# Kernel tuning notes

Measured on AMD Instinct MI355X. Metric: run time of the kernel, lower is better.

## Reference

```python
import jax, jax.numpy as jnp
import numpy as np

N_NODES = 49984   # 32 graphs x 1562 nodes
N_EDGES = 799744  # avg degree 16
DIM_IN = 64
WIDTH = 256
DEPTH = 3         # depth+1 = 4 GCNConv blocks
N_GRAPHS = 32
NODES_PER_GRAPH = 1562


def setup_inputs() -> dict:
    key = jax.random.key(0)
    ks = jax.random.split(key, 12)
    nb = DEPTH + 1
    s_f = 1.0 / np.sqrt(DIM_IN)
    s_g = 1.0 / np.sqrt(WIDTH)
    return {
        "x": jax.random.normal(ks[0], (N_NODES, DIM_IN), dtype=jnp.float32),
        "edge_index": jax.random.randint(ks[1], (2, N_EDGES), 0, N_NODES, dtype=jnp.int32),
        "center": jax.random.randint(ks[2], (N_GRAPHS,), 0, NODES_PER_GRAPH, dtype=jnp.int32),
        "ptr": jnp.arange(N_GRAPHS + 1, dtype=jnp.int32) * NODES_PER_GRAPH,
        # foot: Conv1d(dim_input, width, 1) == per-node linear
        "Wf": jax.random.uniform(ks[3], (WIDTH, DIM_IN), jnp.float32, -s_f, s_f),
        "bf": jax.random.uniform(ks[4], (WIDTH,), jnp.float32, -s_f, s_f),
        # stacked GCNConv params: weight [nb, width, width] (in->out), bias [nb, width]
        "Wg": jax.random.uniform(ks[5], (nb, WIDTH, WIDTH), jnp.float32, -s_g, s_g),
        "bg": jax.random.uniform(ks[6], (nb, WIDTH), jnp.float32, -s_g, s_g),
        # head: Conv1d(width, 7, 1)
        "Wh": jax.random.uniform(ks[7], (7, WIDTH), jnp.float32, -s_g, s_g),
        "bh": jax.random.uniform(ks[8], (7,), jnp.float32, -s_g, s_g),
    }


def reference(x, edge_index, center, ptr, Wf, bf, Wg, bg, Wh, bh):
    N = x.shape[0]
    # foot: 1x1 conv (per-node linear) + exact GELU; dropout = identity (eval)
    h = jax.nn.gelu(x @ Wf.T + bf, approximate=False)  # [N, W]

    # gcn_norm with self-loops (same for every layer since edges are static)
    loops = jnp.arange(N, dtype=edge_index.dtype)
    row = jnp.concatenate([edge_index[0], loops])  # source
    col = jnp.concatenate([edge_index[1], loops])  # target
    deg = jax.ops.segment_sum(jnp.ones_like(row, dtype=h.dtype), col, num_segments=N)
    dis = jnp.where(deg > 0, jax.lax.rsqrt(jnp.maximum(deg, 1.0)), 0.0)
    norm = dis[row] * dis[col]  # [E+N]

    for l in range(Wg.shape[0]):
        xl = h @ Wg[l]                                   # [N, W] linear transform
        msg = xl[row] * norm[:, None]                    # gather + edge scale
        agg = jax.ops.segment_sum(msg, col, num_segments=N) + bg[l]
        h = h + agg                                      # residual

    out = jax.nn.gelu(h, approximate=False) @ Wh.T + bh  # [N, 7]
    return out[center + ptr[:-1]]                        # [B, 7]
```

## Files before the change

### kernel.cpp

```cpp
#include <hip/hip_runtime.h>
#include <math.h>

#define WIDTH 256
typedef unsigned short u16;
typedef unsigned int u32;
typedef __attribute__((ext_vector_type(4))) float f32x4;
typedef __attribute__((ext_vector_type(8))) short bf16x8;

__device__ __forceinline__ float gelu_exact(float v) {
    return 0.5f * v * (1.0f + erff(v * 0.70710678118654752f));
}
__device__ __forceinline__ u16 f2b(float x) {
    u32 u = __builtin_bit_cast(u32, x);
    return (u16)((u + 0x7fffu + ((u >> 16) & 1u)) >> 16);
}
__device__ __forceinline__ float b2f_lo(u32 v) {
    return __builtin_bit_cast(float, v << 16);
}
__device__ __forceinline__ float b2f_hi(u32 v) {
    return __builtin_bit_cast(float, v & 0xffff0000u);
}
__device__ __forceinline__ float b2fu(u16 b) {
    return __builtin_bit_cast(float, ((u32)b) << 16);
}
__device__ __forceinline__ u32 pack2(float a, float b) {
    return (u32)f2b(a) | ((u32)f2b(b) << 16);
}

#define PREP_WG   (4 * 65536)
#define PREP_WF   (256 * 64)
__global__ void k_prep(const float* __restrict__ Wg, const float* __restrict__ Wf,
                       const float* __restrict__ x,
                       u16* __restrict__ WgT, u16* __restrict__ WfT,
                       u16* __restrict__ xb, int total8) {
    int idx = blockIdx.x * blockDim.x + threadIdx.x;
    if (idx < PREP_WG) {
        int l = idx >> 16;
        int k = (idx >> 8) & 255;
        int n = idx & 255;
        WgT[(size_t)l * 65536 + (size_t)n * 256 + k] = f2b(Wg[idx]);
    } else if (idx < PREP_WG + PREP_WF) {
        int j = idx - PREP_WG;
        WfT[j] = f2b(Wf[j]);
    } else if (idx < PREP_WG + PREP_WF + total8) {
        int i = idx - (PREP_WG + PREP_WF);
        const float4 v0 = *reinterpret_cast<const float4*>(&x[(size_t)i * 8]);
        const float4 v1 = *reinterpret_cast<const float4*>(&x[(size_t)i * 8 + 4]);
        uint4 o;
        o.x = pack2(v0.x, v0.y);
        o.y = pack2(v0.z, v0.w);
        o.z = pack2(v1.x, v1.y);
        o.w = pack2(v1.z, v1.w);
        *reinterpret_cast<uint4*>(&xb[(size_t)i * 8]) = o;
    }
}

__global__ void k_hist(const int* __restrict__ col, int* __restrict__ deg,
                       u16* __restrict__ rank, int E) {
    int i = blockIdx.x * blockDim.x + threadIdx.x;
    if (i < E) rank[i] = (u16)atomicAdd(&deg[col[i]], 1);
}

__global__ __launch_bounds__(256) void k_scan1(const int* __restrict__ deg, int* __restrict__ off,
                                               int* __restrict__ part, float* __restrict__ dis, int N) {
    __shared__ int buf[256];
    const int t = threadIdx.x;
    const int gid = blockIdx.x * 256 + t;
    const int v = (gid < N) ? deg[gid] : 0;
    if (gid < N) dis[gid] = rsqrtf(1.0f + (float)v);
    buf[t] = v;
    __syncthreads();
#pragma unroll
    for (int d = 1; d < 256; d <<= 1) {
        int add = (t >= d) ? buf[t - d] : 0;
        __syncthreads();
        buf[t] += add;
        __syncthreads();
    }
    if (gid < N) off[gid] = buf[t] - v;
    if (t == 255) part[blockIdx.x] = buf[255];
}

__global__ __launch_bounds__(256) void k_scan3(int* __restrict__ off, const int* __restrict__ part,
                                               int NB, int N, int E) {
    __shared__ int buf[256];
    const int t = threadIdx.x;
    int v = (t < NB) ? part[t] : 0;
    buf[t] = v;
    __syncthreads();
#pragma unroll
    for (int d = 1; d < 256; d <<= 1) {
        int add = (t >= d) ? buf[t - d] : 0;
        __syncthreads();
        buf[t] += add;
        __syncthreads();
    }
    const int base = (blockIdx.x == 0) ? 0 : buf[blockIdx.x - 1];
    const int gid = blockIdx.x * 256 + t;
    if (gid < N) off[gid] += base;
    if (gid == 0) off[N] = E;
}

__global__ void k_fill(const int* __restrict__ row, const int* __restrict__ col,
                       const u16* __restrict__ rank, const float* __restrict__ dis,
                       const int* __restrict__ off, u32* __restrict__ csr, int E) {
    int i = blockIdx.x * blockDim.x + threadIdx.x;
    if (i < E) {
        const int r = row[i];
        const int pos = off[col[i]] + (int)rank[i];
        csr[pos] = (u32)(u16)r | ((u32)f2b(dis[r]) << 16);
    }
}

__global__ void k_front(const int* __restrict__ center, const int* __restrict__ ptr,
                        const int* __restrict__ off, const u32* __restrict__ csr,
                        int* __restrict__ flags, int* __restrict__ list, int* __restrict__ cnt) {
    const int g = blockIdx.x;
    const int node = center[g] + ptr[g];
    const int t = threadIdx.x;
    const int e0 = off[node];
    const int e1 = off[node + 1];
    if (t == 0) {
        if (atomicExch(&flags[node], 1) == 0) list[atomicAdd(cnt, 1)] = node;
    }
    for (int e = e0 + t; e < e1; e += 256) {
        const int s = (int)(csr[e] & 0xffffu);
        if (atomicExch(&flags[s], 1) == 0) list[atomicAdd(cnt, 1)] = s;
    }
}

template <int KDIM, bool FOOT>
__global__ __launch_bounds__(512) void k_gemm_mfma(const u16* __restrict__ A,
                                                   const u16* __restrict__ BT,
                                                   const float* __restrict__ bias,
                                                   u16* __restrict__ Cb,
                                                   float* __restrict__ Cf, int nrows) {
    __shared__ u16 As[128 * 64];
    __shared__ u16 Bs[256 * 64];

    const int tid = threadIdx.x;
    const int w = tid >> 6;
    const int l = tid & 63;
    const int m0 = blockIdx.x * 128;
    const int wr = w >> 2;
    const int wc = w & 3;

    const int lr = l >> 3;
    const int lc = l & 7;
    const int src_slot = lc ^ lr;

    f32x4 acc[4][4] = {};

#pragma unroll
    for (int ks = 0; ks < KDIM / 64; ++ks) {
        const int k0 = ks * 64;
#pragma unroll
        for (int i = 0; i < 2; ++i) {
            const u16* asrc = A + (size_t)(m0 + 16 * w + 8 * i + lr) * KDIM + k0 + src_slot * 8;
            __builtin_amdgcn_global_load_lds(
                (const __attribute__((address_space(1))) u32*)asrc,
                (__attribute__((address_space(3))) u32*)(As + (16 * w + 8 * i) * 64), 16, 0, 0);
        }
#pragma unroll
        for (int j = 0; j < 4; ++j) {
            const u16* bsrc = BT + (size_t)(32 * w + 8 * j + lr) * KDIM + k0 + src_slot * 8;
            __builtin_amdgcn_global_load_lds(
                (const __attribute__((address_space(1))) u32*)bsrc,
                (__attribute__((address_space(3))) u32*)(Bs + (32 * w + 8 * j) * 64), 16, 0, 0);
        }
        asm volatile("s_waitcnt vmcnt(0)" ::: "memory");
        __syncthreads();

        bf16x8 a[4][2], b[4][2];
#pragma unroll
        for (int fr = 0; fr < 4; ++fr) {
            const int row = 64 * wr + fr * 16 + (l & 15);
#pragma unroll
            for (int kk = 0; kk < 2; ++kk)
                a[fr][kk] = *reinterpret_cast<const bf16x8*>(
                    &As[row * 64 + ((kk * 4 + (l >> 4)) ^ (row & 7)) * 8]);
        }
#pragma unroll
        for (int fc = 0; fc < 4; ++fc) {
            const int row = 64 * wc + fc * 16 + (l & 15);
#pragma unroll
            for (int kk = 0; kk < 2; ++kk)
                b[fc][kk] = *reinterpret_cast<const bf16x8*>(
                    &Bs[row * 64 + ((kk * 4 + (l >> 4)) ^ (row & 7)) * 8]);
        }
#pragma unroll
        for (int fr = 0; fr < 4; ++fr)
#pragma unroll
            for (int fc = 0; fc < 4; ++fc) {
                acc[fr][fc] = __builtin_amdgcn_mfma_f32_16x16x32_bf16(a[fr][0], b[fc][0], acc[fr][fc], 0, 0, 0);
                acc[fr][fc] = __builtin_amdgcn_mfma_f32_16x16x32_bf16(a[fr][1], b[fc][1], acc[fr][fc], 0, 0, 0);
            }
        __syncthreads();
    }

    const int r0 = (l >> 4) * 4;
    const int ci = l & 15;
#pragma unroll
    for (int fr = 0; fr < 4; ++fr)
#pragma unroll
        for (int fc = 0; fc < 4; ++fc) {
            const int col = 64 * wc + fc * 16 + ci;
#pragma unroll
            for (int r = 0; r < 4; ++r) {
                const int row = m0 + 64 * wr + fr * 16 + r0 + r;
                if (row < nrows) {
                    const size_t p = (size_t)row * WIDTH + col;
                    if (FOOT) {
                        const float o = gelu_exact(acc[fr][fc][r] + bias[col]);
                        Cf[p] = o;
                        Cb[p] = f2b(o);
                    } else {
                        Cb[p] = f2b(acc[fr][fc][r]);
                    }
                }
            }
        }
}

#define EDGE_FMA(vv, dd_)                          \
    acc[0] = fmaf(dd_, b2f_lo(vv.x), acc[0]);      \
    acc[1] = fmaf(dd_, b2f_hi(vv.x), acc[1]);      \
    acc[2] = fmaf(dd_, b2f_lo(vv.y), acc[2]);      \
    acc[3] = fmaf(dd_, b2f_hi(vv.y), acc[3]);

__device__ __forceinline__ void agg_node_body(const int* __restrict__ off,
                                              const u32* __restrict__ csr,
                                              const float* __restrict__ dis,
                                              const u16* __restrict__ xlb,
                                              const float* __restrict__ bg,
                                              float* __restrict__ h,
                                              u16* __restrict__ hb,
                                              int node, int hl, int ch0) {
    const int c = ch0 + hl * 4;
    const int e0 = off[node];
    const int e1 = off[node + 1];
    const float di = dis[node];

    float acc[4];
    {
        const uint2 v = *reinterpret_cast<const uint2*>(&xlb[(size_t)node * WIDTH + c]);
        acc[0] = di * b2f_lo(v.x);
        acc[1] = di * b2f_hi(v.x);
        acc[2] = di * b2f_lo(v.y);
        acc[3] = di * b2f_hi(v.y);
    }

    for (int base = e0; base < e1; base += 32) {
        const int m = min(32, e1 - base);
        u32 ep = 0;
        if (hl < m) ep = csr[base + hl];
        int j = 0;
        for (; j + 8 <= m; j += 8) {
            uint2 vv[8];
            float dd[8];
#pragma unroll
            for (int q = 0; q < 8; ++q) {
                const u32 e = (u32)__shfl((int)ep, j + q, 32);
                dd[q] = b2f_hi(e);
                vv[q] = *reinterpret_cast<const uint2*>(&xlb[(size_t)(e & 0xffffu) * WIDTH + c]);
            }
#pragma unroll
            for (int q = 0; q < 8; ++q) { EDGE_FMA(vv[q], dd[q]) }
        }
        if (j + 4 <= m) {
            uint2 vv[4];
            float dd[4];
#pragma unroll
            for (int q = 0; q < 4; ++q) {
                const u32 e = (u32)__shfl((int)ep, j + q, 32);
                dd[q] = b2f_hi(e);
                vv[q] = *reinterpret_cast<const uint2*>(&xlb[(size_t)(e & 0xffffu) * WIDTH + c]);
            }
#pragma unroll
            for (int q = 0; q < 4; ++q) { EDGE_FMA(vv[q], dd[q]) }
            j += 4;
        }
        for (; j < m; ++j) {
            const u32 e = (u32)__shfl((int)ep, j, 32);
            const float dj = b2f_hi(e);
            const uint2 v = *reinterpret_cast<const uint2*>(&xlb[(size_t)(e & 0xffffu) * WIDTH + c]);
            EDGE_FMA(v, dj)
        }
    }

    const size_t p = (size_t)node * WIDTH + c;
    const float4 hv = *reinterpret_cast<const float4*>(&h[p]);
    const float4 bv = *reinterpret_cast<const float4*>(&bg[c]);
    const float o0 = hv.x + bv.x + di * acc[0];
    const float o1 = hv.y + bv.y + di * acc[1];
    const float o2 = hv.z + bv.z + di * acc[2];
    const float o3 = hv.w + bv.w + di * acc[3];
    float4 w0;
    w0.x = o0; w0.y = o1; w0.z = o2; w0.w = o3;
    *reinterpret_cast<float4*>(&h[p]) = w0;
    uint2 ob;
    ob.x = pack2(o0, o1);
    ob.y = pack2(o2, o3);
    *reinterpret_cast<uint2*>(&hb[p]) = ob;
}

__global__ __launch_bounds__(256) void k_agg(const int* __restrict__ off,
                                             const u32* __restrict__ csr,
                                             const float* __restrict__ dis,
                                             const u16* __restrict__ xlb,
                                             const float* __restrict__ bg,
                                             float* __restrict__ h,
                                             u16* __restrict__ hb, int nbh, int N) {
    int bh = blockIdx.x;
    int ch0 = 0;
    if (bh >= nbh) { ch0 = 128; bh -= nbh; }
    const int node = (bh * 256 + threadIdx.x) >> 5;
    if (node >= N) return;
    agg_node_body(off, csr, dis, xlb, bg, h, hb, node, threadIdx.x & 31, ch0);
}

__global__ __launch_bounds__(256) void k_agg_list(const int* __restrict__ off,
                                                  const u32* __restrict__ csr,
                                                  const float* __restrict__ dis,
                                                  const u16* __restrict__ xlb,
                                                  const float* __restrict__ bg,
                                                  float* __restrict__ h,
                                                  u16* __restrict__ hb,
                                                  const int* __restrict__ list,
                                                  const int* __restrict__ cnt) {
    const int nitems = cnt[0] * 2;
    const int hl = threadIdx.x & 31;
    const int stride = (gridDim.x * 256) >> 5;
    for (int item = (blockIdx.x * 256 + threadIdx.x) >> 5; item < nitems; item += stride) {
        const int node = list[item >> 1];
        const int ch0 = (item & 1) << 7;
        agg_node_body(off, csr, dis, xlb, bg, h, hb, node, hl, ch0);
    }
}
#undef EDGE_FMA

__global__ __launch_bounds__(256) void k_tail(const int* __restrict__ off,
                                              const u32* __restrict__ csr,
                                              const float* __restrict__ dis,
                                              const u16* __restrict__ hb,
                                              const float* __restrict__ h,
                                              const float* __restrict__ Wg3,
                                              const float* __restrict__ bg3,
                                              const float* __restrict__ Wh,
                                              const float* __restrict__ bh,
                                              const int* __restrict__ center,
                                              const int* __restrict__ ptr,
                                              float* __restrict__ out) {
    __shared__ float aggK[256];
    __shared__ u32 es[256];
    __shared__ float gs[256];
    const int g = blockIdx.x;
    const int t = threadIdx.x;
    const int node = center[g] + ptr[g];
    const int e0 = off[node];
    const int e1 = off[node + 1];
    const float di = dis[node];

    float acc = di * b2fu(hb[(size_t)node * WIDTH + t]);
    for (int base = e0; base < e1; base += 256) {
        const int m = min(256, e1 - base);
        if (t < m) es[t] = csr[base + t];
        __syncthreads();
        int j = 0;
        for (; j + 4 <= m; j += 4) {
            const u32 a0 = es[j + 0], a1 = es[j + 1], a2 = es[j + 2], a3 = es[j + 3];
            const float v0 = b2fu(hb[(size_t)(a0 & 0xffffu) * WIDTH + t]);
            const float v1 = b2fu(hb[(size_t)(a1 & 0xffffu) * WIDTH + t]);
            const float v2 = b2fu(hb[(size_t)(a2 & 0xffffu) * WIDTH + t]);
            const float v3 = b2fu(hb[(size_t)(a3 & 0xffffu) * WIDTH + t]);
            acc = fmaf(b2f_hi(a0), v0, acc);
            acc = fmaf(b2f_hi(a1), v1, acc);
            acc = fmaf(b2f_hi(a2), v2, acc);
            acc = fmaf(b2f_hi(a3), v3, acc);
        }
        for (; j < m; ++j) {
            const u32 a = es[j];
            acc = fmaf(b2f_hi(a), b2fu(hb[(size_t)(a & 0xffffu) * WIDTH + t]), acc);
        }
        __syncthreads();
    }
    aggK[t] = acc;
    __syncthreads();

    float mv = 0.0f;
#pragma unroll 8
    for (int k = 0; k < 256; ++k)
        mv = fmaf(aggK[k], Wg3[(size_t)k * 256 + t], mv);
    const float h4 = h[(size_t)node * WIDTH + t] + bg3[t] + di * mv;
    gs[t] = gelu_exact(h4);
    __syncthreads();
    if (t < 7) {
        float o = bh[t];
        for (int k = 0; k < 256; ++k)
            o = fmaf(gs[k], Wh[t * 256 + k], o);
        out[g * 7 + t] = o;
    }
}

extern "C" void kernel_launch(void* const* d_in, const int* in_sizes, int n_in,
                              void* d_out, int out_size, void* d_ws, size_t ws_size,
                              hipStream_t stream) {
    const float* x      = (const float*)d_in[0];
    const int*   ei     = (const int*)d_in[1];
    const int*   center = (const int*)d_in[2];
    const int*   ptr    = (const int*)d_in[3];
    const float* Wf     = (const float*)d_in[4];
    const float* bf     = (const float*)d_in[5];
    const float* Wg     = (const float*)d_in[6];
    const float* bg     = (const float*)d_in[7];
    const float* Wh     = (const float*)d_in[8];
    const float* bh     = (const float*)d_in[9];

    const int E = in_sizes[1] / 2;
    const int N = in_sizes[0] / 64;
    const int B = in_sizes[2];

    char* ws = (char*)d_ws;
    size_t o = 0;
    float* h       = (float*)(ws + o); o += (size_t)N * WIDTH * 4;
    u16*   hb      = (u16*)  (ws + o); o += (size_t)N * WIDTH * 2;
    u16*   xlb     = (u16*)  (ws + o); o += (size_t)N * WIDTH * 2;
    u16*   xb      = (u16*)  (ws + o); o += (size_t)N * 64 * 2;
    float* dis     = (float*)(ws + o); o += (size_t)N * 4;
    int*   deg     = (int*)  (ws + o); o += (size_t)N * 4;
    int*   off     = (int*)  (ws + o); o += (size_t)(N + 1) * 4;
    int*   part    = (int*)  (ws + o); o += 1024;
    u16*   rank    = (u16*)  (ws + o); o += (size_t)E * 2;
    u32*   csr     = (u32*)  (ws + o); o += (size_t)E * 4;
    u16*   WgT     = (u16*)  (ws + o); o += (size_t)4 * 65536 * 2;
    u16*   WfT     = (u16*)  (ws + o); o += (size_t)256 * 64 * 2;
    int*   flags   = (int*)  (ws + o); o += (size_t)N * 4;
    int*   cnt     = (int*)  (ws + o); o += 256;
    int*   list    = (int*)  (ws + o); o += (size_t)(E + 64) * 4;

    const int* rowv = ei;
    const int* colv = ei + E;

    const int nb = (N + 255) / 256;
    const int eb = (E + 255) / 256;

    hipMemsetAsync(deg, 0, (size_t)N * 4, stream);
    hipMemsetAsync(flags, 0, (size_t)N * 4 + 256, stream);
    const int total8 = N * 64 / 8;
    const int prep_threads = PREP_WG + PREP_WF + total8;
    k_prep<<<(prep_threads + 255) / 256, 256, 0, stream>>>(Wg, Wf, x, WgT, WfT, xb, total8);
    k_hist<<<eb, 256, 0, stream>>>(colv, deg, rank, E);
    k_scan1<<<nb, 256, 0, stream>>>(deg, off, part, dis, N);
    k_scan3<<<nb, 256, 0, stream>>>(off, part, nb, N, E);
    k_fill<<<eb, 256, 0, stream>>>(rowv, colv, rank, dis, off, csr, E);
    k_front<<<B, 256, 0, stream>>>(center, ptr, off, csr, flags, list, cnt);

    const int gb = (N + 127) / 128;
    k_gemm_mfma<64, true><<<gb, 512, 0, stream>>>(xb, WfT, bf, hb, h, N);

    const int nbh = N / 8;
    for (int l = 0; l < 2; ++l) {
        k_gemm_mfma<256, false><<<gb, 512, 0, stream>>>(hb, WgT + (size_t)l * 65536, nullptr, xlb, nullptr, N);
        k_agg<<<2 * nbh, 256, 0, stream>>>(off, csr, dis, xlb, bg + (size_t)l * WIDTH, h, hb, nbh, N);
    }

    k_gemm_mfma<256, false><<<gb, 512, 0, stream>>>(hb, WgT + (size_t)2 * 65536, nullptr, xlb, nullptr, N);
    k_agg_list<<<256, 256, 0, stream>>>(off, csr, dis, xlb, bg + (size_t)2 * WIDTH, h, hb, list, cnt);

    k_tail<<<B, 256, 0, stream>>>(off, csr, dis, hb, h,
                                  Wg + (size_t)3 * 65536, bg + (size_t)3 * WIDTH,
                                  Wh, bh, center, ptr, (float*)d_out);
}
```

Before: 303.0 us.

## Restrict layer-2 aggregation to the two-hop frontier of the center nodes

Adds a second frontier-expansion kernel that collects every node within two hops of the graph centers. The layer-2 aggregation then runs only over that two-hop list instead of all nodes, and layer 3 keeps using the one-hop list. This cuts the full-graph gather/scatter in the middle layer, at the cost of an extra small kernel and atomic list building. The full GEMMs still run over all nodes, so only the aggregation work shrinks. The two-hop set may cover much of the graph at degree 16 (about 32*17*17 nodes), so the saving could be small.

```diff
diff --git a/kernel.cpp b/kernel.cpp
--- a/kernel.cpp
+++ b/kernel.cpp
@@ -129,6 +129,25 @@
     }
 }
 
+__global__ void k_front2(const int* __restrict__ off, const u32* __restrict__ csr,
+                         const int* __restrict__ list1, const int* __restrict__ cnt1,
+                         int* __restrict__ flags2, int* __restrict__ list2, int* __restrict__ cnt2) {
+    const int n1 = cnt1[0];
+    const int t = threadIdx.x;
+    for (int idx = blockIdx.x; idx < n1; idx += gridDim.x) {
+        const int node = list1[idx];
+        if (t == 0) {
+            if (atomicExch(&flags2[node], 1) == 0) list2[atomicAdd(cnt2, 1)] = node;
+        }
+        const int e0 = off[node];
+        const int e1 = off[node + 1];
+        for (int e = e0 + t; e < e1; e += 256) {
+            const int s = (int)(csr[e] & 0xffffu);
+            if (atomicExch(&flags2[s], 1) == 0) list2[atomicAdd(cnt2, 1)] = s;
+        }
+    }
+}
+
 template <int KDIM, bool FOOT>
 __global__ __launch_bounds__(512) void k_gemm_mfma(const u16* __restrict__ A,
                                                    const u16* __restrict__ BT,
@@ -435,8 +454,11 @@
     u16*   WgT     = (u16*)  (ws + o); o += (size_t)4 * 65536 * 2;
     u16*   WfT     = (u16*)  (ws + o); o += (size_t)256 * 64 * 2;
     int*   flags   = (int*)  (ws + o); o += (size_t)N * 4;
-    int*   cnt     = (int*)  (ws + o); o += 256;
-    int*   list    = (int*)  (ws + o); o += (size_t)(E + 64) * 4;
+    int*   flags2  = (int*)  (ws + o); o += (size_t)N * 4;
+    int*   cnt     = (int*)  (ws + o); o += 128;
+    int*   cnt2    = (int*)  (ws + o); o += 128;
+    int*   list1   = (int*)  (ws + o); o += (size_t)N * 4;
+    int*   list2   = (int*)  (ws + o); o += (size_t)N * 4;
 
     const int* rowv = ei;
     const int* colv = ei + E;
@@ -445,7 +467,7 @@
     const int eb = (E + 255) / 256;
 
     hipMemsetAsync(deg, 0, (size_t)N * 4, stream);
-    hipMemsetAsync(flags, 0, (size_t)N * 4 + 256, stream);
+    hipMemsetAsync(flags, 0, (size_t)N * 8 + 256, stream);
     const int total8 = N * 64 / 8;
     const int prep_threads = PREP_WG + PREP_WF + total8;
     k_prep<<<(prep_threads + 255) / 256, 256, 0, stream>>>(Wg, Wf, x, WgT, WfT, xb, total8);
@@ -453,19 +475,21 @@
     k_scan1<<<nb, 256, 0, stream>>>(deg, off, part, dis, N);
     k_scan3<<<nb, 256, 0, stream>>>(off, part, nb, N, E);
     k_fill<<<eb, 256, 0, stream>>>(rowv, colv, rank, dis, off, csr, E);
-    k_front<<<B, 256, 0, stream>>>(center, ptr, off, csr, flags, list, cnt);
+    k_front<<<B, 256, 0, stream>>>(center, ptr, off, csr, flags, list1, cnt);
+    k_front2<<<64, 256, 0, stream>>>(off, csr, list1, cnt, flags2, list2, cnt2);
 
     const int gb = (N + 127) / 128;
     k_gemm_mfma<64, true><<<gb, 512, 0, stream>>>(xb, WfT, bf, hb, h, N);
 
     const int nbh = N / 8;
-    for (int l = 0; l < 2; ++l) {
-        k_gemm_mfma<256, false><<<gb, 512, 0, stream>>>(hb, WgT + (size_t)l * 65536, nullptr, xlb, nullptr, N);
-        k_agg<<<2 * nbh, 256, 0, stream>>>(off, csr, dis, xlb, bg + (size_t)l * WIDTH, h, hb, nbh, N);
-    }
+    k_gemm_mfma<256, false><<<gb, 512, 0, stream>>>(hb, WgT, nullptr, xlb, nullptr, N);
+    k_agg<<<2 * nbh, 256, 0, stream>>>(off, csr, dis, xlb, bg, h, hb, nbh, N);
+
+    k_gemm_mfma<256, false><<<gb, 512, 0, stream>>>(hb, WgT + (size_t)1 * 65536, nullptr, xlb, nullptr, N);
+    k_agg_list<<<1024, 256, 0, stream>>>(off, csr, dis, xlb, bg + (size_t)1 * WIDTH, h, hb, list2, cnt2);
 
     k_gemm_mfma<256, false><<<gb, 512, 0, stream>>>(hb, WgT + (size_t)2 * 65536, nullptr, xlb, nullptr, N);
-    k_agg_list<<<256, 256, 0, stream>>>(off, csr, dis, xlb, bg + (size_t)2 * WIDTH, h, hb, list, cnt);
+    k_agg_list<<<256, 256, 0, stream>>>(off, csr, dis, xlb, bg + (size_t)2 * WIDTH, h, hb, list1, cnt);
 
     k_tail<<<B, 256, 0, stream>>>(off, csr, dis, hb, h,
                                   Wg + (size_t)3 * 65536, bg + (size_t)3 * WIDTH,
```

After: 273.3 us. 9.8% less time.
